# Performance work log

Hardware: AMD Instinct MI355X
Metric: run time of the kernel (lower is better)

Reference implementation:

```python
import jax, jax.numpy as jnp
import numpy as np

# Constants derived from quantiles=[0.1..0.9] (deciles), df = 9.
QUANTILES = jnp.array([0.1, 0.2, 0.3, 0.4, 0.5, 0.6, 0.7, 0.8, 0.9], dtype=jnp.float32)
# scipy.stats.norm.ppf(quantiles), cast to float32 as in the torch module
Z_SCORES = jnp.array([-1.2815516, -0.8416212, -0.5244005, -0.2533471, 0.0,
                      0.2533471, 0.5244005, 0.8416212, 1.2815516], dtype=jnp.float32)
# expected bin probabilities: q0, diffs, 1-q_last -> all 0.1 for deciles
EXPECTED_PCT = jnp.full((10,), 0.1, dtype=jnp.float32)
# chi2.ppf(1 - p, df=9) for p in QUANTILES (precomputed with scipy offline)
CRIT = jnp.array([14.683657, 12.242145, 10.656372, 9.413640, 8.342832,
                  7.357034, 6.393306, 5.380053, 4.168159], dtype=jnp.float32)
MAX_CRIT = 14.683657
SHARPNESS = 100.0  # sigmoid steepness for the soft histogram


def setup_inputs() -> dict:
    key = jax.random.key(0)
    x = jax.random.normal(key, (16777216,), dtype=jnp.float32)
    return {"x": x}


def reference(x):
    n = x.shape[0]
    mean = x.mean()
    std = jnp.std(x, ddof=1)  # torch.std uses Bessel's correction
    z = (x - mean) / std  # [n]
    # soft cumulative counts at each quantile threshold: [K]
    cum = jax.nn.sigmoid(SHARPNESS * (Z_SCORES[:, None] - z[None, :])).sum(axis=1)
    # bin counts: first cum, consecutive diffs, remainder n - last cum -> [K+1]
    actual = jnp.concatenate([cum[:1], jnp.diff(cum),
                              jnp.asarray(n, z.dtype)[None] - cum[-1:]])
    expected = n * EXPECTED_PCT
    chi2_stat = jnp.sum((actual - expected) ** 2 / (expected + 1e-7))
    # differentiable interpolation of p-value
    w = jax.nn.softmax(-jnp.abs(chi2_stat - CRIT))
    p_value_estimate = 1.0 - jnp.sum(w * QUANTILES)
    excess = jax.nn.relu((chi2_stat - MAX_CRIT) / 100.0)
    return p_value_estimate + excess
```

## Files before the change

kernel.cpp:

```cpp
#include <hip/hip_runtime.h>
#include <math.h>


#if __has_builtin(__builtin_amdgcn_exp2f)
#define EXP2F(x) __builtin_amdgcn_exp2f(x)
#else
#define EXP2F(x) exp2f(x)
#endif
#if __has_builtin(__builtin_amdgcn_rcpf)
#define RCPF(x) __builtin_amdgcn_rcpf(x)
#else
#define RCPF(x) (1.0f / (x))
#endif

#define NBLK 256
#define ABLOCK 1024
#define NBINS 8192

static __device__ __forceinline__ double wave_reduce_d(double v) {
#pragma unroll
    for (int off = 32; off > 0; off >>= 1) v += __shfl_down(v, off);
    return v;
}

__device__ __constant__ double d_ZS[9] = {
    -1.2815516, -0.8416212, -0.5244005, -0.2533471, 0.0,
    0.2533471,  0.5244005,  0.8416212,  1.2815516};

__device__ void epilogue(const double* cum, float* out, int n) {
    const double CRIT[9] = {14.683657, 12.242145, 10.656372, 9.413640, 8.342832,
                            7.357034,  6.393306,  5.380053,  4.168159};
    const double nd = (double)n;
    double actual[10];
    actual[0] = cum[0];
#pragma unroll
    for (int k = 1; k < 9; ++k) actual[k] = cum[k] - cum[k - 1];
    actual[9] = nd - cum[8];
    const double expected = nd * (double)0.1f;
    const double denom = expected + 1e-7;
    double chi2 = 0.0;
#pragma unroll
    for (int j = 0; j < 10; ++j) {
        double d = actual[j] - expected;
        chi2 += d * d / denom;
    }
    double dneg[9], m = -1e300;
#pragma unroll
    for (int k = 0; k < 9; ++k) {
        dneg[k] = -fabs(chi2 - CRIT[k]);
        if (dneg[k] > m) m = dneg[k];
    }
    double W = 0.0, PQ = 0.0;
#pragma unroll
    for (int k = 0; k < 9; ++k) {
        double w = exp(dneg[k] - m);
        W += w;
        PQ += w * (0.1 * (double)(k + 1));
    }
    double p = 1.0 - PQ / W;
    double excess = (chi2 - 14.683657) / 100.0;
    if (excess < 0.0) excess = 0.0;
    out[0] = (float)(p + excess);
}

__global__ __launch_bounds__(ABLOCK) void pass_hist(const float* __restrict__ x,
                                                    double* __restrict__ part1,
                                                    unsigned int* __restrict__ histp,
                                                    int n) {
    __shared__ unsigned int hist[NBINS];
    const int tx = threadIdx.x;
#pragma unroll
    for (int j = 0; j < NBINS / ABLOCK; ++j) hist[tx + j * ABLOCK] = 0u;
    __syncthreads();

    float fs = 0.f, fss = 0.f;
    auto process = [&](float v) {
        fs += v;
        fss = fmaf(v, v, fss);
        int b = (int)fmaf(v, 512.0f, 4096.0f);
        b = b < 0 ? 0 : (b > NBINS - 1 ? NBINS - 1 : b);
        atomicAdd(&hist[b], 1u);
    };

    const int tid = blockIdx.x * ABLOCK + tx;
    const int nthreads = NBLK * ABLOCK;
    const int n4 = n >> 2;
    const float4* __restrict__ x4 = (const float4*)x;
    for (int i = tid; i < n4; i += nthreads) {
        float4 v = x4[i];
        process(v.x); process(v.y); process(v.z); process(v.w);
    }
    if (blockIdx.x == 0 && tx == 0) {
        for (int j = n4 << 2; j < n; ++j) process(x[j]);
    }
    __syncthreads();

#pragma unroll
    for (int j = 0; j < NBINS / ABLOCK; ++j) {
        const int b = tx + j * ABLOCK;
        histp[blockIdx.x * NBINS + b] = hist[b];
    }

    double s = wave_reduce_d((double)fs);
    double ss = wave_reduce_d((double)fss);
    __shared__ double sm[16][2];
    const int lane = tx & 63, wid = tx >> 6;
    if (lane == 0) { sm[wid][0] = s; sm[wid][1] = ss; }
    __syncthreads();
    if (tx == 0) {
        double ts = 0.0, tss = 0.0;
#pragma unroll
        for (int w = 0; w < 16; ++w) { ts += sm[w][0]; tss += sm[w][1]; }
        part1[2 * blockIdx.x] = ts;
        part1[2 * blockIdx.x + 1] = tss;
    }
}

__global__ __launch_bounds__(256) void reduce_hist(const unsigned int* __restrict__ histp,
                                                   unsigned int* __restrict__ H) {
    const int g = blockIdx.x * 256 + threadIdx.x;
    unsigned int a0 = 0, a1 = 0, a2 = 0, a3 = 0;
    for (int b = 0; b < NBLK; b += 4) {
        a0 += histp[(b + 0) * NBINS + g];
        a1 += histp[(b + 1) * NBINS + g];
        a2 += histp[(b + 2) * NBINS + g];
        a3 += histp[(b + 3) * NBINS + g];
    }
    H[g] = (a0 + a1) + (a2 + a3);
}

__global__ __launch_bounds__(ABLOCK) void finalize_kernel(
    const double* __restrict__ part1, const unsigned int* __restrict__ H,
    float* __restrict__ out, int n) {
    const int tx = threadIdx.x;
    const int lane = tx & 63, wid = tx >> 6;
    __shared__ double sm[16][9];
    __shared__ double sMV[2];

    double s = 0.0, ss = 0.0;
    if (tx < NBLK) { s = part1[2 * tx]; ss = part1[2 * tx + 1]; }
    double rs = wave_reduce_d(s);
    double rss = wave_reduce_d(ss);
    if (lane == 0) { sm[wid][0] = rs; sm[wid][1] = rss; }
    __syncthreads();
    if (tx == 0) {
        double ts = 0.0, tss = 0.0;
#pragma unroll
        for (int w = 0; w < 16; ++w) { ts += sm[w][0]; tss += sm[w][1]; }
        const double nd = (double)n;
        const double mean = ts / nd;
        const double var = (tss - ts * ts / nd) / (nd - 1.0);
        sMV[0] = mean;
        sMV[1] = 1.0 / sqrt(var);
    }
    __syncthreads();
    const double mu = sMV[0], isig = sMV[1];
    const double Ld = 144.26950408889634;
    const double wz = (1.0 / 512.0) * isig;
    const double wz2_12 = wz * wz / 12.0;
    const double hgl = wz * 0.28867513459481287;

    double acc[9];
#pragma unroll
    for (int k = 0; k < 9; ++k) acc[k] = 0.0;

    for (int b = tx; b < NBINS; b += ABLOCK) {
        const unsigned int h = H[b];
        if (h == 0u) continue;
        const double dh = (double)h;
        const double c = (double)b * (1.0 / 512.0) + (0.5 / 512.0 - 8.0);
        const double zc = (c - mu) * isig;
        const double zctr = zc - zc * wz2_12;
        const double z1 = zctr - hgl, z2 = zctr + hgl;
#pragma unroll
        for (int k = 0; k < 9; ++k) {
            const float t1 = EXP2F((float)(Ld * (z1 - d_ZS[k])));
            const float t2 = EXP2F((float)(Ld * (z2 - d_ZS[k])));
            const double sg =
                0.5 * ((double)RCPF(1.0f + t1) + (double)RCPF(1.0f + t2));
            acc[k] += dh * sg;
        }
    }

    __syncthreads();
#pragma unroll
    for (int k = 0; k < 9; ++k) {
        double r = wave_reduce_d(acc[k]);
        if (lane == 0) sm[wid][k] = r;
    }
    __syncthreads();
    if (tx == 0) {
        double cum[9];
#pragma unroll
        for (int k = 0; k < 9; ++k) {
            double t = 0.0;
#pragma unroll
            for (int w = 0; w < 16; ++w) t += sm[w][k];
            cum[k] = t;
        }
        epilogue(cum, out, n);
    }
}

extern "C" void kernel_launch(void* const* d_in, const int* in_sizes, int n_in,
                              void* d_out, int out_size, void* d_ws, size_t ws_size,
                              hipStream_t stream) {
    const float* x = (const float*)d_in[0];
    const int n = in_sizes[0];
    double* part1 = (double*)d_ws;
    unsigned int* histp = (unsigned int*)(part1 + 512);
    unsigned int* H = histp + NBLK * NBINS;

    pass_hist<<<NBLK, ABLOCK, 0, stream>>>(x, part1, histp, n);
    reduce_hist<<<32, 256, 0, stream>>>(histp, H);
    finalize_kernel<<<1, ABLOCK, 0, stream>>>(part1, H, (float*)d_out, n);
}
```

Before: 117.9 us.

## Fuse histogram reduction and finalize into main pass via global atomics and last-block ticket

Each block now adds its shared-memory histogram straight into one global histogram with atomics, staggering the starting bin per block, and skips empty bins. The per-block histogram buffer and the separate reduce kernel are gone. A ticket counter picks the last block to finish, and that block computes the statistics and the epilogue, so the finalize kernel is also removed. This saves a write and re-read of 8 MB of partial histograms and one kernel launch. In exchange it adds a small init kernel and contention on the global atomics.

```diff
diff --git a/kernel.cpp b/kernel.cpp
--- a/kernel.cpp
+++ b/kernel.cpp
@@ -63,12 +63,24 @@
     out[0] = (float)(p + excess);
 }
 
-__global__ __launch_bounds__(ABLOCK) void pass_hist(const float* __restrict__ x,
-                                                    double* __restrict__ part1,
-                                                    unsigned int* __restrict__ histp,
-                                                    int n) {
+__global__ __launch_bounds__(ABLOCK) void init_kernel(unsigned int* __restrict__ H,
+                                                      unsigned int* __restrict__ ticket) {
+    const int t = blockIdx.x * ABLOCK + threadIdx.x;
+    if (t < NBINS) H[t] = 0u;
+    if (t == 0) *ticket = 0u;
+}
+
+__global__ __launch_bounds__(ABLOCK) void fused_kernel(
+    const float* __restrict__ x, double* __restrict__ part1,
+    unsigned int* __restrict__ H, unsigned int* __restrict__ ticket,
+    float* __restrict__ out, int n) {
     __shared__ unsigned int hist[NBINS];
+    __shared__ double smd[16][9];
+    __shared__ double sMV[2];
+    __shared__ int sLast;
     const int tx = threadIdx.x;
+    const int lane = tx & 63, wid = tx >> 6;
+
 #pragma unroll
     for (int j = 0; j < NBINS / ABLOCK; ++j) hist[tx + j * ABLOCK] = 0u;
     __syncthreads();
@@ -97,56 +109,53 @@
 
 #pragma unroll
     for (int j = 0; j < NBINS / ABLOCK; ++j) {
-        const int b = tx + j * ABLOCK;
-        histp[blockIdx.x * NBINS + b] = hist[b];
+        const int jj = (j + (int)blockIdx.x) & (NBINS / ABLOCK - 1);
+        const int b = tx + jj * ABLOCK;
+        const unsigned int h = hist[b];
+        if (h) atomicAdd(&H[b], h);
     }
 
     double s = wave_reduce_d((double)fs);
     double ss = wave_reduce_d((double)fss);
-    __shared__ double sm[16][2];
-    const int lane = tx & 63, wid = tx >> 6;
-    if (lane == 0) { sm[wid][0] = s; sm[wid][1] = ss; }
+    if (lane == 0) { smd[wid][0] = s; smd[wid][1] = ss; }
     __syncthreads();
     if (tx == 0) {
         double ts = 0.0, tss = 0.0;
 #pragma unroll
-        for (int w = 0; w < 16; ++w) { ts += sm[w][0]; tss += sm[w][1]; }
-        part1[2 * blockIdx.x] = ts;
-        part1[2 * blockIdx.x + 1] = tss;
-    }
-}
-
-__global__ __launch_bounds__(256) void reduce_hist(const unsigned int* __restrict__ histp,
-                                                   unsigned int* __restrict__ H) {
-    const int g = blockIdx.x * 256 + threadIdx.x;
-    unsigned int a0 = 0, a1 = 0, a2 = 0, a3 = 0;
-    for (int b = 0; b < NBLK; b += 4) {
-        a0 += histp[(b + 0) * NBINS + g];
-        a1 += histp[(b + 1) * NBINS + g];
-        a2 += histp[(b + 2) * NBINS + g];
-        a3 += histp[(b + 3) * NBINS + g];
-    }
-    H[g] = (a0 + a1) + (a2 + a3);
-}
-
-__global__ __launch_bounds__(ABLOCK) void finalize_kernel(
-    const double* __restrict__ part1, const unsigned int* __restrict__ H,
-    float* __restrict__ out, int n) {
-    const int tx = threadIdx.x;
-    const int lane = tx & 63, wid = tx >> 6;
-    __shared__ double sm[16][9];
-    __shared__ double sMV[2];
-
-    double s = 0.0, ss = 0.0;
-    if (tx < NBLK) { s = part1[2 * tx]; ss = part1[2 * tx + 1]; }
-    double rs = wave_reduce_d(s);
-    double rss = wave_reduce_d(ss);
-    if (lane == 0) { sm[wid][0] = rs; sm[wid][1] = rss; }
+        for (int w = 0; w < 16; ++w) { ts += smd[w][0]; tss += smd[w][1]; }
+        __hip_atomic_store(&part1[2 * blockIdx.x], ts, __ATOMIC_RELAXED,
+                           __HIP_MEMORY_SCOPE_AGENT);
+        __hip_atomic_store(&part1[2 * blockIdx.x + 1], tss, __ATOMIC_RELAXED,
+                           __HIP_MEMORY_SCOPE_AGENT);
+    }
+
+    __syncthreads();
+    if (tx == 0) {
+        __threadfence();
+        const unsigned int prev = __hip_atomic_fetch_add(
+            ticket, 1u, __ATOMIC_ACQ_REL, __HIP_MEMORY_SCOPE_AGENT);
+        sLast = (prev == (unsigned int)(NBLK - 1));
+    }
+    __syncthreads();
+    if (!sLast) return;
+    __threadfence();
+
+    double ps = 0.0, pss = 0.0;
+    if (tx < NBLK) {
+        ps = __hip_atomic_load(&part1[2 * tx], __ATOMIC_RELAXED,
+                               __HIP_MEMORY_SCOPE_AGENT);
+        pss = __hip_atomic_load(&part1[2 * tx + 1], __ATOMIC_RELAXED,
+                                __HIP_MEMORY_SCOPE_AGENT);
+    }
+    double rs = wave_reduce_d(ps);
+    double rss = wave_reduce_d(pss);
+    __syncthreads();
+    if (lane == 0) { smd[wid][0] = rs; smd[wid][1] = rss; }
     __syncthreads();
     if (tx == 0) {
         double ts = 0.0, tss = 0.0;
 #pragma unroll
-        for (int w = 0; w < 16; ++w) { ts += sm[w][0]; tss += sm[w][1]; }
+        for (int w = 0; w < 16; ++w) { ts += smd[w][0]; tss += smd[w][1]; }
         const double nd = (double)n;
         const double mean = ts / nd;
         const double var = (tss - ts * ts / nd) / (nd - 1.0);
@@ -165,7 +174,8 @@
     for (int k = 0; k < 9; ++k) acc[k] = 0.0;
 
     for (int b = tx; b < NBINS; b += ABLOCK) {
-        const unsigned int h = H[b];
+        const unsigned int h = __hip_atomic_load(&H[b], __ATOMIC_RELAXED,
+                                                 __HIP_MEMORY_SCOPE_AGENT);
         if (h == 0u) continue;
         const double dh = (double)h;
         const double c = (double)b * (1.0 / 512.0) + (0.5 / 512.0 - 8.0);
@@ -186,7 +196,7 @@
 #pragma unroll
     for (int k = 0; k < 9; ++k) {
         double r = wave_reduce_d(acc[k]);
-        if (lane == 0) sm[wid][k] = r;
+        if (lane == 0) smd[wid][k] = r;
     }
     __syncthreads();
     if (tx == 0) {
@@ -195,7 +205,7 @@
         for (int k = 0; k < 9; ++k) {
             double t = 0.0;
 #pragma unroll
-            for (int w = 0; w < 16; ++w) t += sm[w][k];
+            for (int w = 0; w < 16; ++w) t += smd[w][k];
             cum[k] = t;
         }
         epilogue(cum, out, n);
@@ -208,10 +218,10 @@
     const float* x = (const float*)d_in[0];
     const int n = in_sizes[0];
     double* part1 = (double*)d_ws;
-    unsigned int* histp = (unsigned int*)(part1 + 512);
-    unsigned int* H = histp + NBLK * NBINS;
-
-    pass_hist<<<NBLK, ABLOCK, 0, stream>>>(x, part1, histp, n);
-    reduce_hist<<<32, 256, 0, stream>>>(histp, H);
-    finalize_kernel<<<1, ABLOCK, 0, stream>>>(part1, H, (float*)d_out, n);
-}
+    unsigned int* H = (unsigned int*)(part1 + 512);
+    unsigned int* ticket = H + NBINS;
+
+    init_kernel<<<8, ABLOCK, 0, stream>>>(H, ticket);
+    fused_kernel<<<NBLK, ABLOCK, 0, stream>>>(x, part1, H, ticket,
+                                              (float*)d_out, n);
+}
```

Result: slower. 121.9 us (+3.4%).
